# Kernel tuning notes

Measured on AMD Instinct MI355X. Metric: run time of the kernel, lower is better.

The kernel has to match this reference:

```python
import jax, jax.numpy as jnp
import numpy as np

ALPHA = 0.2  # LeakyReLU negative slope


def setup_inputs() -> dict:
    key = jax.random.key(0)
    k1, k2, k3, k4 = jax.random.split(key, 4)
    B, N, F_IN, F_OUT = 8, 2048, 512, 256
    h = jax.random.normal(k1, (B, N, F_IN), dtype=jnp.float32)
    # torch nn.Linear weights: [out, in]
    W = jax.random.normal(k2, (F_OUT, F_IN), dtype=jnp.float32) * (1.414 / np.sqrt(F_IN))
    a1 = jax.random.normal(k3, (1, F_OUT), dtype=jnp.float32) * (1.414 / np.sqrt(F_OUT))
    a2 = jax.random.normal(k4, (1, F_OUT), dtype=jnp.float32) * (1.414 / np.sqrt(F_OUT))
    return {"h": h, "W": W, "a1": a1, "a2": a2}


def reference(h, W, a1, a2):
    # Wh: [B, N, F_out]
    Wh = jnp.einsum('bnf,of->bno', h, W)
    # additive attention scores
    s1 = jnp.einsum('bno,o->bn', Wh, a1[0])  # [B, N]
    s2 = jnp.einsum('bno,o->bn', Wh, a2[0])  # [B, N]
    e = s1[:, :, None] + s2[:, None, :]       # [B, N, N]
    e = jnp.where(e > 0, e, ALPHA * e)         # LeakyReLU
    attention = jax.nn.softmax(e, axis=2)      # softmax over last dim
    # dropout p=0.0 -> identity
    h_prime = jnp.einsum('bnm,bmo->bno', attention, Wh)
    return jax.nn.elu(h_prime)  # concat=True path
```

## Files before the change

kernel.cpp:

```cpp
#include <hip/hip_runtime.h>

typedef __attribute__((ext_vector_type(8))) _Float16 half8;
typedef __attribute__((ext_vector_type(4))) _Float16 half4;
typedef __attribute__((ext_vector_type(4))) float f32x4;
#if __has_builtin(__builtin_amdgcn_cvt_pkrtz)
typedef __attribute__((ext_vector_type(2))) __fp16 fp16x2;
#endif

#define ALPHA 0.2f
#define LOG2E 1.44269504f

__device__ __forceinline__ void gload_lds16(const void* g, void* l) {
  __builtin_amdgcn_global_load_lds((const __attribute__((address_space(1))) unsigned int*)g,
                                   (__attribute__((address_space(3))) unsigned int*)l, 16, 0, 0);
}

__device__ __forceinline__ float fexp2(float x) {
#if __has_builtin(__builtin_amdgcn_exp2f)
  return __builtin_amdgcn_exp2f(x);
#else
  return __expf(x * 0.69314718f);
#endif
}

__global__ __launch_bounds__(256) void k_convW(const float* __restrict__ W,
                                               _Float16* __restrict__ W16) {
  int idx4 = blockIdx.x * 256 + threadIdx.x;
  int n = idx4 >> 7;
  int q = idx4 & 127;
  float4 v = *reinterpret_cast<const float4*>(W + n * 512 + q * 4);
  half4 hv = {(_Float16)v.x, (_Float16)v.y, (_Float16)v.z, (_Float16)v.w};
  int kp = (q * 4) ^ ((n & 7) << 3);
  *reinterpret_cast<half4*>(W16 + n * 512 + kp) = hv;
}

__global__ __launch_bounds__(256) void k_uvec(const float* __restrict__ W,
                                              const float* __restrict__ a1,
                                              const float* __restrict__ a2,
                                              float* __restrict__ u1,
                                              float* __restrict__ u2) {
  __shared__ float r1[4], r2[4];
  int k = blockIdx.x, t = threadIdx.x;
  float wv = W[t * 512 + k];
  float x1 = wv * a1[t];
  float x2 = wv * a2[t];
#pragma unroll
  for (int off = 32; off >= 1; off >>= 1) {
    x1 += __shfl_xor(x1, off);
    x2 += __shfl_xor(x2, off);
  }
  if ((t & 63) == 0) { r1[t >> 6] = x1; r2[t >> 6] = x2; }
  __syncthreads();
  if (t == 0) {
    u1[k] = r1[0] + r1[1] + r1[2] + r1[3];
    u2[k] = r2[0] + r2[1] + r2[2] + r2[3];
  }
}

__global__ __launch_bounds__(256) void k_smax(const float* __restrict__ s2,
                                              float* __restrict__ smax,
                                              float* __restrict__ s2L) {
  __shared__ float red[4];
  int b = blockIdx.x, t = threadIdx.x;
  float m = -1e30f;
  for (int j = t; j < 2048; j += 256) {
    float v = s2[b * 2048 + j];
    s2L[b * 2048 + j] = LOG2E * v;
    m = fmaxf(m, v);
  }
#pragma unroll
  for (int off = 32; off >= 1; off >>= 1) m = fmaxf(m, __shfl_xor(m, off));
  if ((t & 63) == 0) red[t >> 6] = m;
  __syncthreads();
  if (t == 0) smax[b] = fmaxf(fmaxf(red[0], red[1]), fmaxf(red[2], red[3]));
}

__global__ __launch_bounds__(256) void k_gemm_wh(const float* __restrict__ h,
                                                 const _Float16* __restrict__ W16,
                                                 const float* __restrict__ u1,
                                                 const float* __restrict__ u2,
                                                 float* __restrict__ s1o,
                                                 float* __restrict__ s2o,
                                                 _Float16* __restrict__ WhT) {
  __shared__ _Float16 Ab[2][32 * 64];
  __shared__ _Float16 Bb[2][256 * 64];
  const int t = threadIdx.x, lane = t & 63, w = t >> 6;
  const int i0 = blockIdx.x * 32;
  const int b = i0 >> 11, n0 = i0 & 2047;
  const int ar = t >> 3, au = t & 7;
  const float* hrow = h + (size_t)(i0 + ar) * 512 + au * 8;

  f32x4 acc[2][4];
#pragma unroll
  for (int mi = 0; mi < 2; ++mi)
#pragma unroll
    for (int ni = 0; ni < 4; ++ni) acc[mi][ni] = (f32x4){0.f, 0.f, 0.f, 0.f};

  float4 aR0 = *reinterpret_cast<const float4*>(hrow);
  float4 aR1 = *reinterpret_cast<const float4*>(hrow + 4);
#pragma unroll
  for (int q = 0; q < 8; ++q) {
    int idx = (q * 4 + w) * 64 + lane;
    int nn = idx >> 3, uu = idx & 7;
    gload_lds16(W16 + nn * 512 + uu * 8, (char*)&Bb[0][0] + idx * 16);
  }
  float x1 = 0.f, x2 = 0.f;

  for (int kt = 0; kt < 8; ++kt) {
    const int cur = kt & 1;
    {
      half8 av;
      av[0] = (_Float16)aR0.x; av[1] = (_Float16)aR0.y;
      av[2] = (_Float16)aR0.z; av[3] = (_Float16)aR0.w;
      av[4] = (_Float16)aR1.x; av[5] = (_Float16)aR1.y;
      av[6] = (_Float16)aR1.z; av[7] = (_Float16)aR1.w;
      *reinterpret_cast<half8*>((char*)&Ab[cur][0] + ar * 128 + ((au * 16) ^ ((ar & 7) << 4))) = av;
      const float* up1 = u1 + kt * 64 + au * 8;
      const float* up2 = u2 + kt * 64 + au * 8;
      float4 u1a = *reinterpret_cast<const float4*>(up1);
      float4 u1b = *reinterpret_cast<const float4*>(up1 + 4);
      float4 u2a = *reinterpret_cast<const float4*>(up2);
      float4 u2b = *reinterpret_cast<const float4*>(up2 + 4);
      x1 += aR0.x * u1a.x + aR0.y * u1a.y + aR0.z * u1a.z + aR0.w * u1a.w
          + aR1.x * u1b.x + aR1.y * u1b.y + aR1.z * u1b.z + aR1.w * u1b.w;
      x2 += aR0.x * u2a.x + aR0.y * u2a.y + aR0.z * u2a.z + aR0.w * u2a.w
          + aR1.x * u2b.x + aR1.y * u2b.y + aR1.z * u2b.z + aR1.w * u2b.w;
    }
    __syncthreads();
    if (kt < 7) {
      const int k0 = (kt + 1) * 64;
      aR0 = *reinterpret_cast<const float4*>(hrow + k0);
      aR1 = *reinterpret_cast<const float4*>(hrow + k0 + 4);
#pragma unroll
      for (int q = 0; q < 8; ++q) {
        int idx = (q * 4 + w) * 64 + lane;
        int nn = idx >> 3, uu = idx & 7;
        gload_lds16(W16 + nn * 512 + k0 + uu * 8, (char*)&Bb[cur ^ 1][0] + idx * 16);
      }
    }
    const char* Ac = (const char*)&Ab[cur][0];
    const char* Bc = (const char*)&Bb[cur][0];
#pragma unroll
    for (int kk = 0; kk < 2; ++kk) {
      const int jb = (lane >> 4) * 16 + kk * 64;
      half8 afr[2];
#pragma unroll
      for (int mi = 0; mi < 2; ++mi) {
        int rr = (lane & 15) + 16 * mi;
        afr[mi] = *reinterpret_cast<const half8*>(Ac + rr * 128 + (jb ^ ((rr & 7) << 4)));
      }
#pragma unroll
      for (int ni = 0; ni < 4; ++ni) {
        int nn = 64 * w + 16 * ni + (lane & 15);
        half8 bfr = *reinterpret_cast<const half8*>(Bc + nn * 128 + (jb ^ ((nn & 7) << 4)));
#pragma unroll
        for (int mi = 0; mi < 2; ++mi)
          acc[mi][ni] = __builtin_amdgcn_mfma_f32_16x16x32_f16(afr[mi], bfr, acc[mi][ni], 0, 0, 0);
      }
    }
  }
  x1 += __shfl_xor(x1, 1); x1 += __shfl_xor(x1, 2); x1 += __shfl_xor(x1, 4);
  x2 += __shfl_xor(x2, 1); x2 += __shfl_xor(x2, 2); x2 += __shfl_xor(x2, 4);
  if (au == 0) { s1o[i0 + ar] = x1; s2o[i0 + ar] = x2; }
  _Float16* whtb = WhT + (size_t)b * 256 * 2048;
#pragma unroll
  for (int mi = 0; mi < 2; ++mi)
#pragma unroll
    for (int ni = 0; ni < 4; ++ni) {
      int c = 64 * w + 16 * ni + (lane & 15);
      int nb = n0 + 16 * mi + (lane >> 4) * 4;
      int np = nb ^ ((c & 7) << 3);
      f32x4 a = acc[mi][ni];
      half4 hv = {(_Float16)a[0], (_Float16)a[1], (_Float16)a[2], (_Float16)a[3]};
      *reinterpret_cast<half4*>(whtb + (size_t)c * 2048 + np) = hv;
    }
}

__global__ __launch_bounds__(512) void k_attn(const _Float16* __restrict__ WhT,
                                              const float* __restrict__ s1,
                                              const float* __restrict__ s2L,
                                              const float* __restrict__ smax,
                                              float* __restrict__ out) {
  __shared__ _Float16 Bb[2][256 * 64];
  __shared__ _Float16 Pb[2][32 * 64];
  __shared__ float d_lds[32];
  const int t = threadIdx.x, lane = t & 63, w = t >> 6;
  const int rg = w >> 2, cg = w & 3;
  const int bid = blockIdx.x;
  const int b = bid & 7;
  const int i0 = (bid >> 3) * 32;
  const _Float16* whtb = WhT + (size_t)b * 256 * 2048;
  const float* s2Lb = s2L + b * 2048;
  const int arow = lane & 15;
  const float sm = smax[b];
  const int pr = t >> 4, pj = t & 15;
  const float s1p = s1[b * 2048 + i0 + pr];
  const float e0p = s1p + sm;
  const float mrowp = fmaxf(e0p, ALPHA * e0p);
  const float C1 = LOG2E * (s1p - mrowp);
  const float C2 = fmaf(ALPHA * LOG2E, s1p, -LOG2E * mrowp);
  const int pwoff = pr * 128 + ((pj * 8) ^ ((pr & 7) << 4));
  half8 onesb;
  {
    _Float16 ov = (arow == 0) ? (_Float16)1.0f : (_Float16)0.0f;
#pragma unroll
    for (int x = 0; x < 8; ++x) onesb[x] = ov;
  }
  f32x4 acc[4];
#pragma unroll
  for (int ni = 0; ni < 4; ++ni) acc[ni] = (f32x4){0.f, 0.f, 0.f, 0.f};
  f32x4 accd = (f32x4){0.f, 0.f, 0.f, 0.f};

#pragma unroll
  for (int q = 0; q < 4; ++q) {
    int idx = q * 512 + t;
    int cl = idx >> 3, uu = idx & 7;
    gload_lds16(whtb + (size_t)cl * 2048 + uu * 8, (char*)&Bb[0][0] + idx * 16);
  }
  {
    float4 sv = *reinterpret_cast<const float4*>(s2Lb + pj * 4);
    float p0 = fexp2(fmaxf(C1 + sv.x, fmaf(ALPHA, sv.x, C2)));
    float p1 = fexp2(fmaxf(C1 + sv.y, fmaf(ALPHA, sv.y, C2)));
    float p2 = fexp2(fmaxf(C1 + sv.z, fmaf(ALPHA, sv.z, C2)));
    float p3 = fexp2(fmaxf(C1 + sv.w, fmaf(ALPHA, sv.w, C2)));
    half4 hv;
#if __has_builtin(__builtin_amdgcn_cvt_pkrtz)
    fp16x2 q0 = __builtin_amdgcn_cvt_pkrtz(p0, p1);
    fp16x2 q1 = __builtin_amdgcn_cvt_pkrtz(p2, p3);
    hv[0] = (_Float16)q0[0]; hv[1] = (_Float16)q0[1];
    hv[2] = (_Float16)q1[0]; hv[3] = (_Float16)q1[1];
#else
    hv[0] = (_Float16)p0; hv[1] = (_Float16)p1; hv[2] = (_Float16)p2; hv[3] = (_Float16)p3;
#endif
    *reinterpret_cast<half4*>((char*)&Pb[0][0] + pwoff) = hv;
  }

  for (int jt = 0; jt < 32; ++jt) {
    const int cur = jt & 1;
    __syncthreads();
    if (jt < 31) {
      const int j0n = (jt + 1) * 64;
#pragma unroll
      for (int q = 0; q < 4; ++q) {
        int idx = q * 512 + t;
        int cl = idx >> 3, uu = idx & 7;
        gload_lds16(whtb + (size_t)cl * 2048 + j0n + uu * 8, (char*)&Bb[cur ^ 1][0] + idx * 16);
      }
      float4 sv = *reinterpret_cast<const float4*>(s2Lb + j0n + pj * 4);
      float p0 = fexp2(fmaxf(C1 + sv.x, fmaf(ALPHA, sv.x, C2)));
      float p1 = fexp2(fmaxf(C1 + sv.y, fmaf(ALPHA, sv.y, C2)));
      float p2 = fexp2(fmaxf(C1 + sv.z, fmaf(ALPHA, sv.z, C2)));
      float p3 = fexp2(fmaxf(C1 + sv.w, fmaf(ALPHA, sv.w, C2)));
      half4 hv;
#if __has_builtin(__builtin_amdgcn_cvt_pkrtz)
      fp16x2 q0 = __builtin_amdgcn_cvt_pkrtz(p0, p1);
      fp16x2 q1 = __builtin_amdgcn_cvt_pkrtz(p2, p3);
      hv[0] = (_Float16)q0[0]; hv[1] = (_Float16)q0[1];
      hv[2] = (_Float16)q1[0]; hv[3] = (_Float16)q1[1];
#else
      hv[0] = (_Float16)p0; hv[1] = (_Float16)p1; hv[2] = (_Float16)p2; hv[3] = (_Float16)p3;
#endif
      *reinterpret_cast<half4*>((char*)&Pb[cur ^ 1][0] + pwoff) = hv;
    }
    const char* Bc = (const char*)&Bb[cur][0];
    const char* Pc = (const char*)&Pb[cur][0];
#pragma unroll
    for (int kk = 0; kk < 2; ++kk) {
      const int jb = ((lane >> 4) * 8 + kk * 32) * 2;
      const int ar32 = rg * 16 + arow;
      half8 afr = *reinterpret_cast<const half8*>(Pc + ar32 * 128 + (jb ^ ((ar32 & 7) << 4)));
      if (cg == 0)
        accd = __builtin_amdgcn_mfma_f32_16x16x32_f16(afr, onesb, accd, 0, 0, 0);
#pragma unroll
      for (int ni = 0; ni < 4; ++ni) {
        int cl = cg * 64 + 16 * ni + arow;
        half8 bfr = *reinterpret_cast<const half8*>(Bc + cl * 128 + (jb ^ ((cl & 7) << 4)));
        acc[ni] = __builtin_amdgcn_mfma_f32_16x16x32_f16(afr, bfr, acc[ni], 0, 0, 0);
      }
    }
  }
  if (cg == 0 && arow == 0) {
#pragma unroll
    for (int reg = 0; reg < 4; ++reg)
      d_lds[rg * 16 + (lane >> 4) * 4 + reg] = accd[reg];
  }
  __syncthreads();
  const size_t ob = ((size_t)b * 2048 + i0 + rg * 16) * 256 + cg * 64;
#pragma unroll
  for (int reg = 0; reg < 4; ++reg) {
    int rr = (lane >> 4) * 4 + reg;
    float inv = 1.0f / d_lds[rg * 16 + rr];
#pragma unroll
    for (int ni = 0; ni < 4; ++ni) {
      int c = 16 * ni + arow;
      float v = acc[ni][reg] * inv;
      v = v > 0.f ? v : (__expf(v) - 1.f);
      out[ob + (size_t)rr * 256 + c] = v;
    }
  }
}

extern "C" void kernel_launch(void* const* d_in, const int* in_sizes, int n_in,
                              void* d_out, int out_size, void* d_ws, size_t ws_size,
                              hipStream_t stream) {
  (void)in_sizes; (void)n_in; (void)out_size; (void)ws_size;
  const float* h = (const float*)d_in[0];
  const float* W = (const float*)d_in[1];
  const float* a1 = (const float*)d_in[2];
  const float* a2 = (const float*)d_in[3];
  float* out = (float*)d_out;
  char* ws = (char*)d_ws;
  _Float16* WhT = (_Float16*)(ws);
  _Float16* W16 = (_Float16*)(ws + 8388608);
  float* u1 = (float*)(ws + 8650752);
  float* u2 = (float*)(ws + 8652800);
  float* s1 = (float*)(ws + 8654848);
  float* s2 = (float*)(ws + 8720384);
  float* smax = (float*)(ws + 8785920);
  float* s2L = (float*)(ws + 8785952);

  hipLaunchKernelGGL(k_convW, dim3(128), dim3(256), 0, stream, W, W16);
  hipLaunchKernelGGL(k_uvec, dim3(512), dim3(256), 0, stream, W, a1, a2, u1, u2);
  hipLaunchKernelGGL(k_gemm_wh, dim3(512), dim3(256), 0, stream, h, W16, u1, u2, s1, s2, WhT);
  hipLaunchKernelGGL(k_smax, dim3(8), dim3(256), 0, stream, s2, smax, s2L);
  hipLaunchKernelGGL(k_attn, dim3(512), dim3(512), 0, stream, WhT, s1, s2L, smax, out);
}
```

Before: 70.87 us.

## Triple-buffer GEMM and attention loads, enlarge tiles, fold smax into attention

Both main kernels now use a three-stage LDS ring for the B operand with explicit vmcnt waits and raw barriers, prefetching two tiles ahead. Tiles double to 64 rows per block with 512 and 1024 threads. The separate smax kernel is removed: each attention block reduces max(s2) and stages log2e-scaled s2 in LDS itself. k_uvec is restructured to 8 blocks with coalesced column loads, and u vectors are cached in LDS. The larger LDS footprint and thread counts may reduce occupancy, and the hand-written waitcnt values must match the issued load counts exactly.

```diff
diff --git a/kernel.cpp b/kernel.cpp
--- a/kernel.cpp
+++ b/kernel.cpp
@@ -19,7 +19,7 @@
 #if __has_builtin(__builtin_amdgcn_exp2f)
   return __builtin_amdgcn_exp2f(x);
 #else
-  return __expf(x * 0.69314718f);
+  return exp2f(x);
 #endif
 }
 
@@ -39,119 +39,124 @@
                                               const float* __restrict__ a2,
                                               float* __restrict__ u1,
                                               float* __restrict__ u2) {
-  __shared__ float r1[4], r2[4];
-  int k = blockIdx.x, t = threadIdx.x;
-  float wv = W[t * 512 + k];
-  float x1 = wv * a1[t];
-  float x2 = wv * a2[t];
-#pragma unroll
-  for (int off = 32; off >= 1; off >>= 1) {
-    x1 += __shfl_xor(x1, off);
-    x2 += __shfl_xor(x2, off);
-  }
-  if ((t & 63) == 0) { r1[t >> 6] = x1; r2[t >> 6] = x2; }
+  __shared__ float p1[4][64], p2[4][64];
+  int t = threadIdx.x;
+  int l = t & 63, g = t >> 6;
+  int k = blockIdx.x * 64 + l;
+  float x1 = 0.f, x2 = 0.f;
+  for (int o = g * 64; o < g * 64 + 64; ++o) {
+    float wv = W[o * 512 + k];
+    x1 += wv * a1[o];
+    x2 += wv * a2[o];
+  }
+  p1[g][l] = x1; p2[g][l] = x2;
   __syncthreads();
-  if (t == 0) {
-    u1[k] = r1[0] + r1[1] + r1[2] + r1[3];
-    u2[k] = r2[0] + r2[1] + r2[2] + r2[3];
-  }
-}
-
-__global__ __launch_bounds__(256) void k_smax(const float* __restrict__ s2,
-                                              float* __restrict__ smax,
-                                              float* __restrict__ s2L) {
-  __shared__ float red[4];
-  int b = blockIdx.x, t = threadIdx.x;
-  float m = -1e30f;
-  for (int j = t; j < 2048; j += 256) {
-    float v = s2[b * 2048 + j];
-    s2L[b * 2048 + j] = LOG2E * v;
-    m = fmaxf(m, v);
-  }
-#pragma unroll
-  for (int off = 32; off >= 1; off >>= 1) m = fmaxf(m, __shfl_xor(m, off));
-  if ((t & 63) == 0) red[t >> 6] = m;
-  __syncthreads();
-  if (t == 0) smax[b] = fmaxf(fmaxf(red[0], red[1]), fmaxf(red[2], red[3]));
-}
-
-__global__ __launch_bounds__(256) void k_gemm_wh(const float* __restrict__ h,
+  if (g == 0) {
+    u1[k] = p1[0][l] + p1[1][l] + p1[2][l] + p1[3][l];
+    u2[k] = p2[0][l] + p2[1][l] + p2[2][l] + p2[3][l];
+  }
+}
+
+__global__ __launch_bounds__(512) void k_gemm_wh(const float* __restrict__ h,
                                                  const _Float16* __restrict__ W16,
                                                  const float* __restrict__ u1,
                                                  const float* __restrict__ u2,
                                                  float* __restrict__ s1o,
                                                  float* __restrict__ s2o,
                                                  _Float16* __restrict__ WhT) {
-  __shared__ _Float16 Ab[2][32 * 64];
-  __shared__ _Float16 Bb[2][256 * 64];
+  __shared__ _Float16 Ab[2][64 * 64];
+  __shared__ _Float16 Bb[3][256 * 64];
+  __shared__ float u_lds[1024];
   const int t = threadIdx.x, lane = t & 63, w = t >> 6;
-  const int i0 = blockIdx.x * 32;
+  const int rg = w >> 2, cg = w & 3;
+  const int i0 = blockIdx.x * 64;
   const int b = i0 >> 11, n0 = i0 & 2047;
   const int ar = t >> 3, au = t & 7;
+  const int arow = lane & 15;
   const float* hrow = h + (size_t)(i0 + ar) * 512 + au * 8;
+  const int awoff = ar * 128 + ((au * 16) ^ ((ar & 7) << 4));
+
+  u_lds[t] = u1[t];
+  u_lds[512 + t] = u2[t];
+  __syncthreads();
 
   f32x4 acc[2][4];
 #pragma unroll
   for (int mi = 0; mi < 2; ++mi)
 #pragma unroll
     for (int ni = 0; ni < 4; ++ni) acc[mi][ni] = (f32x4){0.f, 0.f, 0.f, 0.f};
-
-  float4 aR0 = *reinterpret_cast<const float4*>(hrow);
-  float4 aR1 = *reinterpret_cast<const float4*>(hrow + 4);
-#pragma unroll
-  for (int q = 0; q < 8; ++q) {
-    int idx = (q * 4 + w) * 64 + lane;
-    int nn = idx >> 3, uu = idx & 7;
-    gload_lds16(W16 + nn * 512 + uu * 8, (char*)&Bb[0][0] + idx * 16);
-  }
   float x1 = 0.f, x2 = 0.f;
 
+  float4 aRx[2], aRy[2];
+  aRx[0] = *reinterpret_cast<const float4*>(hrow);
+  aRy[0] = *reinterpret_cast<const float4*>(hrow + 4);
+#pragma unroll
+  for (int x = 0; x < 2; ++x)
+#pragma unroll
+    for (int q = 0; q < 4; ++q) {
+      int idx = q * 512 + t;
+      int cl = idx >> 3, uu = idx & 7;
+      gload_lds16(W16 + cl * 512 + x * 64 + uu * 8, (char*)&Bb[x][0] + idx * 16);
+    }
+  aRx[1] = *reinterpret_cast<const float4*>(hrow + 64);
+  aRy[1] = *reinterpret_cast<const float4*>(hrow + 68);
+  {
+    float4 a0 = aRx[0], a1v = aRy[0];
+    half8 av;
+    av[0] = (_Float16)a0.x; av[1] = (_Float16)a0.y; av[2] = (_Float16)a0.z; av[3] = (_Float16)a0.w;
+    av[4] = (_Float16)a1v.x; av[5] = (_Float16)a1v.y; av[6] = (_Float16)a1v.z; av[7] = (_Float16)a1v.w;
+    *reinterpret_cast<half8*>((char*)&Ab[0][0] + awoff) = av;
+    const float* up1 = &u_lds[au * 8];
+    const float* up2 = &u_lds[512 + au * 8];
+    x1 += a0.x * up1[0] + a0.y * up1[1] + a0.z * up1[2] + a0.w * up1[3]
+        + a1v.x * up1[4] + a1v.y * up1[5] + a1v.z * up1[6] + a1v.w * up1[7];
+    x2 += a0.x * up2[0] + a0.y * up2[1] + a0.z * up2[2] + a0.w * up2[3]
+        + a1v.x * up2[4] + a1v.y * up2[5] + a1v.z * up2[6] + a1v.w * up2[7];
+  }
+
+#pragma unroll
   for (int kt = 0; kt < 8; ++kt) {
-    const int cur = kt & 1;
-    {
+    asm volatile("s_waitcnt vmcnt(6) lgkmcnt(0)" ::: "memory");
+    __builtin_amdgcn_s_barrier();
+    if (kt < 6) {
+      const int k0 = (kt + 2) * 64;
+      const int p = (kt + 2) % 3;
+#pragma unroll
+      for (int q = 0; q < 4; ++q) {
+        int idx = q * 512 + t;
+        int cl = idx >> 3, uu = idx & 7;
+        gload_lds16(W16 + cl * 512 + k0 + uu * 8, (char*)&Bb[p][0] + idx * 16);
+      }
+      aRx[kt & 1] = *reinterpret_cast<const float4*>(hrow + k0);
+      aRy[kt & 1] = *reinterpret_cast<const float4*>(hrow + k0 + 4);
+    }
+    if (kt < 7) {
+      float4 a0 = aRx[(kt + 1) & 1], a1v = aRy[(kt + 1) & 1];
       half8 av;
-      av[0] = (_Float16)aR0.x; av[1] = (_Float16)aR0.y;
-      av[2] = (_Float16)aR0.z; av[3] = (_Float16)aR0.w;
-      av[4] = (_Float16)aR1.x; av[5] = (_Float16)aR1.y;
-      av[6] = (_Float16)aR1.z; av[7] = (_Float16)aR1.w;
-      *reinterpret_cast<half8*>((char*)&Ab[cur][0] + ar * 128 + ((au * 16) ^ ((ar & 7) << 4))) = av;
-      const float* up1 = u1 + kt * 64 + au * 8;
-      const float* up2 = u2 + kt * 64 + au * 8;
-      float4 u1a = *reinterpret_cast<const float4*>(up1);
-      float4 u1b = *reinterpret_cast<const float4*>(up1 + 4);
-      float4 u2a = *reinterpret_cast<const float4*>(up2);
-      float4 u2b = *reinterpret_cast<const float4*>(up2 + 4);
-      x1 += aR0.x * u1a.x + aR0.y * u1a.y + aR0.z * u1a.z + aR0.w * u1a.w
-          + aR1.x * u1b.x + aR1.y * u1b.y + aR1.z * u1b.z + aR1.w * u1b.w;
-      x2 += aR0.x * u2a.x + aR0.y * u2a.y + aR0.z * u2a.z + aR0.w * u2a.w
-          + aR1.x * u2b.x + aR1.y * u2b.y + aR1.z * u2b.z + aR1.w * u2b.w;
-    }
-    __syncthreads();
-    if (kt < 7) {
-      const int k0 = (kt + 1) * 64;
-      aR0 = *reinterpret_cast<const float4*>(hrow + k0);
-      aR1 = *reinterpret_cast<const float4*>(hrow + k0 + 4);
-#pragma unroll
-      for (int q = 0; q < 8; ++q) {
-        int idx = (q * 4 + w) * 64 + lane;
-        int nn = idx >> 3, uu = idx & 7;
-        gload_lds16(W16 + nn * 512 + k0 + uu * 8, (char*)&Bb[cur ^ 1][0] + idx * 16);
-      }
-    }
-    const char* Ac = (const char*)&Ab[cur][0];
-    const char* Bc = (const char*)&Bb[cur][0];
+      av[0] = (_Float16)a0.x; av[1] = (_Float16)a0.y; av[2] = (_Float16)a0.z; av[3] = (_Float16)a0.w;
+      av[4] = (_Float16)a1v.x; av[5] = (_Float16)a1v.y; av[6] = (_Float16)a1v.z; av[7] = (_Float16)a1v.w;
+      *reinterpret_cast<half8*>((char*)&Ab[(kt + 1) & 1][0] + awoff) = av;
+      const float* up1 = &u_lds[(kt + 1) * 64 + au * 8];
+      const float* up2 = &u_lds[512 + (kt + 1) * 64 + au * 8];
+      x1 += a0.x * up1[0] + a0.y * up1[1] + a0.z * up1[2] + a0.w * up1[3]
+          + a1v.x * up1[4] + a1v.y * up1[5] + a1v.z * up1[6] + a1v.w * up1[7];
+      x2 += a0.x * up2[0] + a0.y * up2[1] + a0.z * up2[2] + a0.w * up2[3]
+          + a1v.x * up2[4] + a1v.y * up2[5] + a1v.z * up2[6] + a1v.w * up2[7];
+    }
+    const char* Ac = (const char*)&Ab[kt & 1][0];
+    const char* Bc = (const char*)&Bb[kt % 3][0];
 #pragma unroll
     for (int kk = 0; kk < 2; ++kk) {
-      const int jb = (lane >> 4) * 16 + kk * 64;
+      const int jb = ((lane >> 4) * 8 + kk * 32) * 2;
       half8 afr[2];
 #pragma unroll
       for (int mi = 0; mi < 2; ++mi) {
-        int rr = (lane & 15) + 16 * mi;
+        int rr = rg * 32 + 16 * mi + arow;
         afr[mi] = *reinterpret_cast<const half8*>(Ac + rr * 128 + (jb ^ ((rr & 7) << 4)));
       }
 #pragma unroll
       for (int ni = 0; ni < 4; ++ni) {
-        int nn = 64 * w + 16 * ni + (lane & 15);
+        int nn = cg * 64 + 16 * ni + arow;
         half8 bfr = *reinterpret_cast<const half8*>(Bc + nn * 128 + (jb ^ ((nn & 7) << 4)));
 #pragma unroll
         for (int mi = 0; mi < 2; ++mi)
@@ -167,8 +172,8 @@
   for (int mi = 0; mi < 2; ++mi)
 #pragma unroll
     for (int ni = 0; ni < 4; ++ni) {
-      int c = 64 * w + 16 * ni + (lane & 15);
-      int nb = n0 + 16 * mi + (lane >> 4) * 4;
+      int c = cg * 64 + 16 * ni + arow;
+      int nb = n0 + rg * 32 + 16 * mi + (lane >> 4) * 4;
       int np = nb ^ ((c & 7) << 3);
       f32x4 a = acc[mi][ni];
       half4 hv = {(_Float16)a[0], (_Float16)a[1], (_Float16)a[2], (_Float16)a[3]};
@@ -176,29 +181,43 @@
     }
 }
 
-__global__ __launch_bounds__(512) void k_attn(const _Float16* __restrict__ WhT,
-                                              const float* __restrict__ s1,
-                                              const float* __restrict__ s2L,
-                                              const float* __restrict__ smax,
-                                              float* __restrict__ out) {
-  __shared__ _Float16 Bb[2][256 * 64];
-  __shared__ _Float16 Pb[2][32 * 64];
-  __shared__ float d_lds[32];
+__global__ __launch_bounds__(1024) void k_attn(const _Float16* __restrict__ WhT,
+                                               const float* __restrict__ s1,
+                                               const float* __restrict__ s2,
+                                               float* __restrict__ out) {
+  __shared__ _Float16 Bb[3][256 * 64];
+  __shared__ _Float16 Pb[2][64 * 64];
+  __shared__ float s2s[2048];
+  __shared__ float red[16];
+  __shared__ float d_lds[64];
   const int t = threadIdx.x, lane = t & 63, w = t >> 6;
   const int rg = w >> 2, cg = w & 3;
-  const int bid = blockIdx.x;
-  const int b = bid & 7;
-  const int i0 = (bid >> 3) * 32;
+  const int b = blockIdx.x & 7;
+  const int i0 = (blockIdx.x >> 3) * 64;
   const _Float16* whtb = WhT + (size_t)b * 256 * 2048;
-  const float* s2Lb = s2L + b * 2048;
   const int arow = lane & 15;
-  const float sm = smax[b];
   const int pr = t >> 4, pj = t & 15;
-  const float s1p = s1[b * 2048 + i0 + pr];
-  const float e0p = s1p + sm;
-  const float mrowp = fmaxf(e0p, ALPHA * e0p);
-  const float C1 = LOG2E * (s1p - mrowp);
-  const float C2 = fmaf(ALPHA * LOG2E, s1p, -LOG2E * mrowp);
+  const float s1v = s1[b * 2048 + i0 + pr];
+
+  float2 sv2 = *reinterpret_cast<const float2*>(s2 + b * 2048 + t * 2);
+  float m0 = fmaxf(sv2.x, sv2.y);
+  *reinterpret_cast<float2*>(&s2s[t * 2]) = make_float2(sv2.x * LOG2E, sv2.y * LOG2E);
+#pragma unroll
+  for (int off = 32; off >= 1; off >>= 1) m0 = fmaxf(m0, __shfl_xor(m0, off));
+  if (lane == 0) red[w] = m0;
+  __syncthreads();
+  float smaxL;
+  {
+    float mm = red[0];
+#pragma unroll
+    for (int i = 1; i < 16; ++i) mm = fmaxf(mm, red[i]);
+    smaxL = mm * LOG2E;
+  }
+  const float s1L = LOG2E * s1v;
+  const float e0L = s1L + smaxL;
+  const float mrowL = fmaxf(e0L, ALPHA * e0L);
+  const float C1 = s1L - mrowL;
+  const float C2 = fmaf(ALPHA, s1L, -mrowL);
   const int pwoff = pr * 128 + ((pj * 8) ^ ((pr & 7) << 4));
   half8 onesb;
   {
@@ -211,14 +230,8 @@
   for (int ni = 0; ni < 4; ++ni) acc[ni] = (f32x4){0.f, 0.f, 0.f, 0.f};
   f32x4 accd = (f32x4){0.f, 0.f, 0.f, 0.f};
 
-#pragma unroll
-  for (int q = 0; q < 4; ++q) {
-    int idx = q * 512 + t;
-    int cl = idx >> 3, uu = idx & 7;
-    gload_lds16(whtb + (size_t)cl * 2048 + uu * 8, (char*)&Bb[0][0] + idx * 16);
-  }
   {
-    float4 sv = *reinterpret_cast<const float4*>(s2Lb + pj * 4);
+    float4 sv = *reinterpret_cast<const float4*>(&s2s[pj * 4]);
     float p0 = fexp2(fmaxf(C1 + sv.x, fmaf(ALPHA, sv.x, C2)));
     float p1 = fexp2(fmaxf(C1 + sv.y, fmaf(ALPHA, sv.y, C2)));
     float p2 = fexp2(fmaxf(C1 + sv.z, fmaf(ALPHA, sv.z, C2)));
@@ -234,19 +247,31 @@
 #endif
     *reinterpret_cast<half4*>((char*)&Pb[0][0] + pwoff) = hv;
   }
+#pragma unroll
+  for (int x = 0; x < 2; ++x)
+#pragma unroll
+    for (int q = 0; q < 2; ++q) {
+      int idx = q * 1024 + t;
+      int cl = idx >> 3, uu = idx & 7;
+      gload_lds16(whtb + (size_t)cl * 2048 + x * 64 + uu * 8, (char*)&Bb[x][0] + idx * 16);
+    }
 
   for (int jt = 0; jt < 32; ++jt) {
-    const int cur = jt & 1;
-    __syncthreads();
+    if (jt < 31) asm volatile("s_waitcnt vmcnt(2) lgkmcnt(0)" ::: "memory");
+    else         asm volatile("s_waitcnt vmcnt(0) lgkmcnt(0)" ::: "memory");
+    __builtin_amdgcn_s_barrier();
+    if (jt < 30) {
+      const int j0n = (jt + 2) * 64;
+      const int p = (jt + 2) % 3;
+#pragma unroll
+      for (int q = 0; q < 2; ++q) {
+        int idx = q * 1024 + t;
+        int cl = idx >> 3, uu = idx & 7;
+        gload_lds16(whtb + (size_t)cl * 2048 + j0n + uu * 8, (char*)&Bb[p][0] + idx * 16);
+      }
+    }
     if (jt < 31) {
-      const int j0n = (jt + 1) * 64;
-#pragma unroll
-      for (int q = 0; q < 4; ++q) {
-        int idx = q * 512 + t;
-        int cl = idx >> 3, uu = idx & 7;
-        gload_lds16(whtb + (size_t)cl * 2048 + j0n + uu * 8, (char*)&Bb[cur ^ 1][0] + idx * 16);
-      }
-      float4 sv = *reinterpret_cast<const float4*>(s2Lb + j0n + pj * 4);
+      float4 sv = *reinterpret_cast<const float4*>(&s2s[(jt + 1) * 64 + pj * 4]);
       float p0 = fexp2(fmaxf(C1 + sv.x, fmaf(ALPHA, sv.x, C2)));
       float p1 = fexp2(fmaxf(C1 + sv.y, fmaf(ALPHA, sv.y, C2)));
       float p2 = fexp2(fmaxf(C1 + sv.z, fmaf(ALPHA, sv.z, C2)));
@@ -260,15 +285,15 @@
 #else
       hv[0] = (_Float16)p0; hv[1] = (_Float16)p1; hv[2] = (_Float16)p2; hv[3] = (_Float16)p3;
 #endif
-      *reinterpret_cast<half4*>((char*)&Pb[cur ^ 1][0] + pwoff) = hv;
-    }
-    const char* Bc = (const char*)&Bb[cur][0];
-    const char* Pc = (const char*)&Pb[cur][0];
+      *reinterpret_cast<half4*>((char*)&Pb[(jt + 1) & 1][0] + pwoff) = hv;
+    }
+    const char* Bc = (const char*)&Bb[jt % 3][0];
+    const char* Pc = (const char*)&Pb[jt & 1][0];
 #pragma unroll
     for (int kk = 0; kk < 2; ++kk) {
       const int jb = ((lane >> 4) * 8 + kk * 32) * 2;
-      const int ar32 = rg * 16 + arow;
-      half8 afr = *reinterpret_cast<const half8*>(Pc + ar32 * 128 + (jb ^ ((ar32 & 7) << 4)));
+      const int ar64 = rg * 16 + arow;
+      half8 afr = *reinterpret_cast<const half8*>(Pc + ar64 * 128 + (jb ^ ((ar64 & 7) << 4)));
       if (cg == 0)
         accd = __builtin_amdgcn_mfma_f32_16x16x32_f16(afr, onesb, accd, 0, 0, 0);
 #pragma unroll
@@ -316,12 +341,9 @@
   float* u2 = (float*)(ws + 8652800);
   float* s1 = (float*)(ws + 8654848);
   float* s2 = (float*)(ws + 8720384);
-  float* smax = (float*)(ws + 8785920);
-  float* s2L = (float*)(ws + 8785952);
 
   hipLaunchKernelGGL(k_convW, dim3(128), dim3(256), 0, stream, W, W16);
-  hipLaunchKernelGGL(k_uvec, dim3(512), dim3(256), 0, stream, W, a1, a2, u1, u2);
-  hipLaunchKernelGGL(k_gemm_wh, dim3(512), dim3(256), 0, stream, h, W16, u1, u2, s1, s2, WhT);
-  hipLaunchKernelGGL(k_smax, dim3(8), dim3(256), 0, stream, s2, smax, s2L);
-  hipLaunchKernelGGL(k_attn, dim3(512), dim3(512), 0, stream, WhT, s1, s2L, smax, out);
-}
+  hipLaunchKernelGGL(k_uvec, dim3(8), dim3(256), 0, stream, W, a1, a2, u1, u2);
+  hipLaunchKernelGGL(k_gemm_wh, dim3(256), dim3(512), 0, stream, h, W16, u1, u2, s1, s2, WhT);
+  hipLaunchKernelGGL(k_attn, dim3(256), dim3(1024), 0, stream, WhT, s1, s2, out);
+}
```

New measurement: 71.85 us. Within noise of the previous version (+1.4%).

## Fuse smax into attention, use 32x32 MFMA, 64-row tiles, triple-buffered loads

Applied to the files above, without the earlier changes.

The attention kernel now takes 64 query rows per block, using 32x32x16 MFMA instead of 16x16x32. It computes the per-batch s2 max and scaled s2 in LDS itself, which removes the separate smax kernel and its launch. WhT tiles are triple-buffered with explicit waitcnt and barrier, so loads run two tiles ahead. k_uvec is restructured to 8 blocks with coalesced column loops. The cost is higher LDS use, which may cut occupancy, and only 256 blocks on the grid.

```diff
diff --git a/kernel.cpp b/kernel.cpp
--- a/kernel.cpp
+++ b/kernel.cpp
@@ -3,6 +3,7 @@
 typedef __attribute__((ext_vector_type(8))) _Float16 half8;
 typedef __attribute__((ext_vector_type(4))) _Float16 half4;
 typedef __attribute__((ext_vector_type(4))) float f32x4;
+typedef __attribute__((ext_vector_type(16))) float f32x16;
 #if __has_builtin(__builtin_amdgcn_cvt_pkrtz)
 typedef __attribute__((ext_vector_type(2))) __fp16 fp16x2;
 #endif
@@ -19,7 +20,7 @@
 #if __has_builtin(__builtin_amdgcn_exp2f)
   return __builtin_amdgcn_exp2f(x);
 #else
-  return __expf(x * 0.69314718f);
+  return exp2f(x);
 #endif
 }
 
@@ -39,40 +40,22 @@
                                               const float* __restrict__ a2,
                                               float* __restrict__ u1,
                                               float* __restrict__ u2) {
-  __shared__ float r1[4], r2[4];
-  int k = blockIdx.x, t = threadIdx.x;
-  float wv = W[t * 512 + k];
-  float x1 = wv * a1[t];
-  float x2 = wv * a2[t];
-#pragma unroll
-  for (int off = 32; off >= 1; off >>= 1) {
-    x1 += __shfl_xor(x1, off);
-    x2 += __shfl_xor(x2, off);
-  }
-  if ((t & 63) == 0) { r1[t >> 6] = x1; r2[t >> 6] = x2; }
+  __shared__ float p1[4][64], p2[4][64];
+  int t = threadIdx.x;
+  int l = t & 63, g = t >> 6;
+  int k = blockIdx.x * 64 + l;
+  float x1 = 0.f, x2 = 0.f;
+  for (int o = g * 64; o < g * 64 + 64; ++o) {
+    float wv = W[o * 512 + k];
+    x1 += wv * a1[o];
+    x2 += wv * a2[o];
+  }
+  p1[g][l] = x1; p2[g][l] = x2;
   __syncthreads();
-  if (t == 0) {
-    u1[k] = r1[0] + r1[1] + r1[2] + r1[3];
-    u2[k] = r2[0] + r2[1] + r2[2] + r2[3];
-  }
-}
-
-__global__ __launch_bounds__(256) void k_smax(const float* __restrict__ s2,
-                                              float* __restrict__ smax,
-                                              float* __restrict__ s2L) {
-  __shared__ float red[4];
-  int b = blockIdx.x, t = threadIdx.x;
-  float m = -1e30f;
-  for (int j = t; j < 2048; j += 256) {
-    float v = s2[b * 2048 + j];
-    s2L[b * 2048 + j] = LOG2E * v;
-    m = fmaxf(m, v);
-  }
-#pragma unroll
-  for (int off = 32; off >= 1; off >>= 1) m = fmaxf(m, __shfl_xor(m, off));
-  if ((t & 63) == 0) red[t >> 6] = m;
-  __syncthreads();
-  if (t == 0) smax[b] = fmaxf(fmaxf(red[0], red[1]), fmaxf(red[2], red[3]));
+  if (g == 0) {
+    u1[k] = p1[0][l] + p1[1][l] + p1[2][l] + p1[3][l];
+    u2[k] = p2[0][l] + p2[1][l] + p2[2][l] + p2[3][l];
+  }
 }
 
 __global__ __launch_bounds__(256) void k_gemm_wh(const float* __restrict__ h,
@@ -178,124 +161,168 @@
 
 __global__ __launch_bounds__(512) void k_attn(const _Float16* __restrict__ WhT,
                                               const float* __restrict__ s1,
-                                              const float* __restrict__ s2L,
-                                              const float* __restrict__ smax,
+                                              const float* __restrict__ s2,
                                               float* __restrict__ out) {
-  __shared__ _Float16 Bb[2][256 * 64];
-  __shared__ _Float16 Pb[2][32 * 64];
-  __shared__ float d_lds[32];
+  __shared__ _Float16 Bb[3][256 * 64];
+  __shared__ _Float16 Pb[2][64 * 64];
+  __shared__ float s2s[2048];
+  __shared__ float red[8];
+  __shared__ float d_lds[64];
   const int t = threadIdx.x, lane = t & 63, w = t >> 6;
   const int rg = w >> 2, cg = w & 3;
-  const int bid = blockIdx.x;
-  const int b = bid & 7;
-  const int i0 = (bid >> 3) * 32;
+  const int b = blockIdx.x & 7;
+  const int i0 = (blockIdx.x >> 3) * 64;
   const _Float16* whtb = WhT + (size_t)b * 256 * 2048;
-  const float* s2Lb = s2L + b * 2048;
-  const int arow = lane & 15;
-  const float sm = smax[b];
-  const int pr = t >> 4, pj = t & 15;
-  const float s1p = s1[b * 2048 + i0 + pr];
-  const float e0p = s1p + sm;
-  const float mrowp = fmaxf(e0p, ALPHA * e0p);
-  const float C1 = LOG2E * (s1p - mrowp);
-  const float C2 = fmaf(ALPHA * LOG2E, s1p, -LOG2E * mrowp);
-  const int pwoff = pr * 128 + ((pj * 8) ^ ((pr & 7) << 4));
+  const int pr = t >> 3, pj8 = t & 7;
+  const float s1v = s1[b * 2048 + i0 + pr];
+
+  float4 sv4 = *reinterpret_cast<const float4*>(s2 + b * 2048 + t * 4);
+  float m0 = fmaxf(fmaxf(sv4.x, sv4.y), fmaxf(sv4.z, sv4.w));
+  *reinterpret_cast<float4*>(&s2s[t * 4]) =
+      make_float4(sv4.x * LOG2E, sv4.y * LOG2E, sv4.z * LOG2E, sv4.w * LOG2E);
+#pragma unroll
+  for (int off = 32; off >= 1; off >>= 1) m0 = fmaxf(m0, __shfl_xor(m0, off));
+  if (lane == 0) red[w] = m0;
+  __syncthreads();
+  float smaxL;
+  {
+    float mm = red[0];
+#pragma unroll
+    for (int i = 1; i < 8; ++i) mm = fmaxf(mm, red[i]);
+    smaxL = mm * LOG2E;
+  }
+  const float s1L = LOG2E * s1v;
+  const float e0L = s1L + smaxL;
+  const float mrowL = fmaxf(e0L, ALPHA * e0L);
+  const float C1 = s1L - mrowL;
+  const float C2 = fmaf(ALPHA, s1L, -mrowL);
+  const int pwoff = pr * 128 + ((pj8 * 16) ^ ((pr & 7) << 4));
   half8 onesb;
   {
-    _Float16 ov = (arow == 0) ? (_Float16)1.0f : (_Float16)0.0f;
+    _Float16 ov = ((lane & 31) == 0) ? (_Float16)1.0f : (_Float16)0.0f;
 #pragma unroll
     for (int x = 0; x < 8; ++x) onesb[x] = ov;
   }
-  f32x4 acc[4];
-#pragma unroll
-  for (int ni = 0; ni < 4; ++ni) acc[ni] = (f32x4){0.f, 0.f, 0.f, 0.f};
-  f32x4 accd = (f32x4){0.f, 0.f, 0.f, 0.f};
-
-#pragma unroll
-  for (int q = 0; q < 4; ++q) {
-    int idx = q * 512 + t;
-    int cl = idx >> 3, uu = idx & 7;
-    gload_lds16(whtb + (size_t)cl * 2048 + uu * 8, (char*)&Bb[0][0] + idx * 16);
-  }
+  f32x16 acc[2];
+  acc[0] = (f32x16)(0.f);
+  acc[1] = (f32x16)(0.f);
+  f32x16 accd = (f32x16)(0.f);
+
   {
-    float4 sv = *reinterpret_cast<const float4*>(s2Lb + pj * 4);
-    float p0 = fexp2(fmaxf(C1 + sv.x, fmaf(ALPHA, sv.x, C2)));
-    float p1 = fexp2(fmaxf(C1 + sv.y, fmaf(ALPHA, sv.y, C2)));
-    float p2 = fexp2(fmaxf(C1 + sv.z, fmaf(ALPHA, sv.z, C2)));
-    float p3 = fexp2(fmaxf(C1 + sv.w, fmaf(ALPHA, sv.w, C2)));
-    half4 hv;
+    float4 sa = *reinterpret_cast<const float4*>(&s2s[pj8 * 8]);
+    float4 sb = *reinterpret_cast<const float4*>(&s2s[pj8 * 8 + 4]);
+    float p0 = fexp2(fmaxf(C1 + sa.x, fmaf(ALPHA, sa.x, C2)));
+    float p1 = fexp2(fmaxf(C1 + sa.y, fmaf(ALPHA, sa.y, C2)));
+    float p2 = fexp2(fmaxf(C1 + sa.z, fmaf(ALPHA, sa.z, C2)));
+    float p3 = fexp2(fmaxf(C1 + sa.w, fmaf(ALPHA, sa.w, C2)));
+    float p4 = fexp2(fmaxf(C1 + sb.x, fmaf(ALPHA, sb.x, C2)));
+    float p5 = fexp2(fmaxf(C1 + sb.y, fmaf(ALPHA, sb.y, C2)));
+    float p6 = fexp2(fmaxf(C1 + sb.z, fmaf(ALPHA, sb.z, C2)));
+    float p7 = fexp2(fmaxf(C1 + sb.w, fmaf(ALPHA, sb.w, C2)));
+    half8 ph;
 #if __has_builtin(__builtin_amdgcn_cvt_pkrtz)
     fp16x2 q0 = __builtin_amdgcn_cvt_pkrtz(p0, p1);
     fp16x2 q1 = __builtin_amdgcn_cvt_pkrtz(p2, p3);
-    hv[0] = (_Float16)q0[0]; hv[1] = (_Float16)q0[1];
-    hv[2] = (_Float16)q1[0]; hv[3] = (_Float16)q1[1];
+    fp16x2 q2 = __builtin_amdgcn_cvt_pkrtz(p4, p5);
+    fp16x2 q3 = __builtin_amdgcn_cvt_pkrtz(p6, p7);
+    ph[0] = (_Float16)q0[0]; ph[1] = (_Float16)q0[1];
+    ph[2] = (_Float16)q1[0]; ph[3] = (_Float16)q1[1];
+    ph[4] = (_Float16)q2[0]; ph[5] = (_Float16)q2[1];
+    ph[6] = (_Float16)q3[0]; ph[7] = (_Float16)q3[1];
 #else
-    hv[0] = (_Float16)p0; hv[1] = (_Float16)p1; hv[2] = (_Float16)p2; hv[3] = (_Float16)p3;
+    ph[0] = (_Float16)p0; ph[1] = (_Float16)p1; ph[2] = (_Float16)p2; ph[3] = (_Float16)p3;
+    ph[4] = (_Float16)p4; ph[5] = (_Float16)p5; ph[6] = (_Float16)p6; ph[7] = (_Float16)p7;
 #endif
-    *reinterpret_cast<half4*>((char*)&Pb[0][0] + pwoff) = hv;
-  }
+    *reinterpret_cast<half8*>((char*)&Pb[0][0] + pwoff) = ph;
+  }
+#pragma unroll
+  for (int x = 0; x < 2; ++x)
+#pragma unroll
+    for (int q = 0; q < 4; ++q) {
+      int idx = q * 512 + t;
+      int cl = idx >> 3, uu = idx & 7;
+      gload_lds16(whtb + (size_t)cl * 2048 + x * 64 + uu * 8, (char*)&Bb[x][0] + idx * 16);
+    }
 
   for (int jt = 0; jt < 32; ++jt) {
-    const int cur = jt & 1;
-    __syncthreads();
-    if (jt < 31) {
-      const int j0n = (jt + 1) * 64;
+    if (jt < 31) asm volatile("s_waitcnt vmcnt(4) lgkmcnt(0)" ::: "memory");
+    else         asm volatile("s_waitcnt vmcnt(0) lgkmcnt(0)" ::: "memory");
+    __builtin_amdgcn_s_barrier();
+    if (jt < 30) {
+      const int j0n = (jt + 2) * 64;
+      const int p = (jt + 2) % 3;
 #pragma unroll
       for (int q = 0; q < 4; ++q) {
         int idx = q * 512 + t;
         int cl = idx >> 3, uu = idx & 7;
-        gload_lds16(whtb + (size_t)cl * 2048 + j0n + uu * 8, (char*)&Bb[cur ^ 1][0] + idx * 16);
-      }
-      float4 sv = *reinterpret_cast<const float4*>(s2Lb + j0n + pj * 4);
-      float p0 = fexp2(fmaxf(C1 + sv.x, fmaf(ALPHA, sv.x, C2)));
-      float p1 = fexp2(fmaxf(C1 + sv.y, fmaf(ALPHA, sv.y, C2)));
-      float p2 = fexp2(fmaxf(C1 + sv.z, fmaf(ALPHA, sv.z, C2)));
-      float p3 = fexp2(fmaxf(C1 + sv.w, fmaf(ALPHA, sv.w, C2)));
-      half4 hv;
+        gload_lds16(whtb + (size_t)cl * 2048 + j0n + uu * 8, (char*)&Bb[p][0] + idx * 16);
+      }
+    }
+    if (jt < 31) {
+      const int j0n = (jt + 1) * 64;
+      float4 sa = *reinterpret_cast<const float4*>(&s2s[j0n + pj8 * 8]);
+      float4 sb = *reinterpret_cast<const float4*>(&s2s[j0n + pj8 * 8 + 4]);
+      float p0 = fexp2(fmaxf(C1 + sa.x, fmaf(ALPHA, sa.x, C2)));
+      float p1 = fexp2(fmaxf(C1 + sa.y, fmaf(ALPHA, sa.y, C2)));
+      float p2 = fexp2(fmaxf(C1 + sa.z, fmaf(ALPHA, sa.z, C2)));
+      float p3 = fexp2(fmaxf(C1 + sa.w, fmaf(ALPHA, sa.w, C2)));
+      float p4 = fexp2(fmaxf(C1 + sb.x, fmaf(ALPHA, sb.x, C2)));
+      float p5 = fexp2(fmaxf(C1 + sb.y, fmaf(ALPHA, sb.y, C2)));
+      float p6 = fexp2(fmaxf(C1 + sb.z, fmaf(ALPHA, sb.z, C2)));
+      float p7 = fexp2(fmaxf(C1 + sb.w, fmaf(ALPHA, sb.w, C2)));
+      half8 ph;
 #if __has_builtin(__builtin_amdgcn_cvt_pkrtz)
       fp16x2 q0 = __builtin_amdgcn_cvt_pkrtz(p0, p1);
       fp16x2 q1 = __builtin_amdgcn_cvt_pkrtz(p2, p3);
-      hv[0] = (_Float16)q0[0]; hv[1] = (_Float16)q0[1];
-      hv[2] = (_Float16)q1[0]; hv[3] = (_Float16)q1[1];
+      fp16x2 q2 = __builtin_amdgcn_cvt_pkrtz(p4, p5);
+      fp16x2 q3 = __builtin_amdgcn_cvt_pkrtz(p6, p7);
+      ph[0] = (_Float16)q0[0]; ph[1] = (_Float16)q0[1];
+      ph[2] = (_Float16)q1[0]; ph[3] = (_Float16)q1[1];
+      ph[4] = (_Float16)q2[0]; ph[5] = (_Float16)q2[1];
+      ph[6] = (_Float16)q3[0]; ph[7] = (_Float16)q3[1];
 #else
-      hv[0] = (_Float16)p0; hv[1] = (_Float16)p1; hv[2] = (_Float16)p2; hv[3] = (_Float16)p3;
+      ph[0] = (_Float16)p0; ph[1] = (_Float16)p1; ph[2] = (_Float16)p2; ph[3] = (_Float16)p3;
+      ph[4] = (_Float16)p4; ph[5] = (_Float16)p5; ph[6] = (_Float16)p6; ph[7] = (_Float16)p7;
 #endif
-      *reinterpret_cast<half4*>((char*)&Pb[cur ^ 1][0] + pwoff) = hv;
-    }
-    const char* Bc = (const char*)&Bb[cur][0];
-    const char* Pc = (const char*)&Pb[cur][0];
-#pragma unroll
-    for (int kk = 0; kk < 2; ++kk) {
-      const int jb = ((lane >> 4) * 8 + kk * 32) * 2;
-      const int ar32 = rg * 16 + arow;
-      half8 afr = *reinterpret_cast<const half8*>(Pc + ar32 * 128 + (jb ^ ((ar32 & 7) << 4)));
+      *reinterpret_cast<half8*>((char*)&Pb[(jt + 1) & 1][0] + pwoff) = ph;
+    }
+    const char* Bc = (const char*)&Bb[jt % 3][0];
+    const char* Pc = (const char*)&Pb[jt & 1][0];
+    const int r32 = rg * 32 + (lane & 31);
+    const int khalf = (lane >> 5) * 16;
+#pragma unroll
+    for (int ks = 0; ks < 4; ++ks) {
+      const int jb = ks * 32 + khalf;
+      half8 afr = *reinterpret_cast<const half8*>(Pc + r32 * 128 + (jb ^ ((r32 & 7) << 4)));
       if (cg == 0)
-        accd = __builtin_amdgcn_mfma_f32_16x16x32_f16(afr, onesb, accd, 0, 0, 0);
-#pragma unroll
-      for (int ni = 0; ni < 4; ++ni) {
-        int cl = cg * 64 + 16 * ni + arow;
+        accd = __builtin_amdgcn_mfma_f32_32x32x16_f16(afr, onesb, accd, 0, 0, 0);
+#pragma unroll
+      for (int ni = 0; ni < 2; ++ni) {
+        int cl = cg * 64 + ni * 32 + (lane & 31);
         half8 bfr = *reinterpret_cast<const half8*>(Bc + cl * 128 + (jb ^ ((cl & 7) << 4)));
-        acc[ni] = __builtin_amdgcn_mfma_f32_16x16x32_f16(afr, bfr, acc[ni], 0, 0, 0);
-      }
-    }
-  }
-  if (cg == 0 && arow == 0) {
-#pragma unroll
-    for (int reg = 0; reg < 4; ++reg)
-      d_lds[rg * 16 + (lane >> 4) * 4 + reg] = accd[reg];
+        acc[ni] = __builtin_amdgcn_mfma_f32_32x32x16_f16(afr, bfr, acc[ni], 0, 0, 0);
+      }
+    }
+  }
+  if (cg == 0 && (lane & 31) == 0) {
+#pragma unroll
+    for (int reg = 0; reg < 16; ++reg) {
+      int rr = rg * 32 + (reg & 3) + 8 * (reg >> 2) + 4 * (lane >> 5);
+      d_lds[rr] = 1.0f / accd[reg];
+    }
   }
   __syncthreads();
-  const size_t ob = ((size_t)b * 2048 + i0 + rg * 16) * 256 + cg * 64;
-#pragma unroll
-  for (int reg = 0; reg < 4; ++reg) {
-    int rr = (lane >> 4) * 4 + reg;
-    float inv = 1.0f / d_lds[rg * 16 + rr];
-#pragma unroll
-    for (int ni = 0; ni < 4; ++ni) {
-      int c = 16 * ni + arow;
+  const int col = cg * 64 + (lane & 31);
+#pragma unroll
+  for (int reg = 0; reg < 16; ++reg) {
+    int rr = rg * 32 + (reg & 3) + 8 * (reg >> 2) + 4 * (lane >> 5);
+    float inv = d_lds[rr];
+    size_t obase = ((size_t)b * 2048 + i0 + rr) * 256 + col;
+#pragma unroll
+    for (int ni = 0; ni < 2; ++ni) {
       float v = acc[ni][reg] * inv;
       v = v > 0.f ? v : (__expf(v) - 1.f);
-      out[ob + (size_t)rr * 256 + c] = v;
+      out[obase + ni * 32] = v;
     }
   }
 }
@@ -316,12 +343,9 @@
   float* u2 = (float*)(ws + 8652800);
   float* s1 = (float*)(ws + 8654848);
   float* s2 = (float*)(ws + 8720384);
-  float* smax = (float*)(ws + 8785920);
-  float* s2L = (float*)(ws + 8785952);
 
   hipLaunchKernelGGL(k_convW, dim3(128), dim3(256), 0, stream, W, W16);
-  hipLaunchKernelGGL(k_uvec, dim3(512), dim3(256), 0, stream, W, a1, a2, u1, u2);
+  hipLaunchKernelGGL(k_uvec, dim3(8), dim3(256), 0, stream, W, a1, a2, u1, u2);
   hipLaunchKernelGGL(k_gemm_wh, dim3(512), dim3(256), 0, stream, h, W16, u1, u2, s1, s2, WhT);
-  hipLaunchKernelGGL(k_smax, dim3(8), dim3(256), 0, stream, s2, smax, s2L);
-  hipLaunchKernelGGL(k_attn, dim3(512), dim3(512), 0, stream, WhT, s1, s2L, smax, out);
-}
+  hipLaunchKernelGGL(k_attn, dim3(256), dim3(512), 0, stream, WhT, s1, s2, out);
+}
```

Result: slower. 75.73 us (+6.9%).
